# Kernel tuning notes

Measured on AMD Instinct MI355X. Metric: run time of the kernel, lower is better.

## Reference

```python
import jax, jax.numpy as jnp
import numpy as np

D_MODEL = 2048
N_HEADS = 16
HEAD_DIM = D_MODEL // N_HEADS  # 128
B, T = 2, 1024
XL_LEN = 1024


def setup_inputs() -> dict:
    key = jax.random.key(0)
    ks = jax.random.split(key, 8)
    # rotary angles for head_dim/2 pairs (llama-style)
    inv_freq = 1.0 / (10000.0 ** (jnp.arange(0, HEAD_DIM, 2, dtype=jnp.float32) / HEAD_DIM))
    t = jnp.arange(T, dtype=jnp.float32)
    freqs = jnp.outer(t, inv_freq)  # [T, HEAD_DIM//2]
    return {
        "x": jax.random.normal(ks[0], (B, T, D_MODEL), dtype=jnp.float32),
        "cos": jnp.cos(freqs),
        "sin": jnp.sin(freqs),
        "k_xl": jax.random.normal(ks[1], (B, XL_LEN, D_MODEL), dtype=jnp.float32),
        "v_xl": jax.random.normal(ks[2], (B, XL_LEN, D_MODEL), dtype=jnp.float32),
        "pos_emb": jax.random.normal(ks[3], (XL_LEN, D_MODEL), dtype=jnp.float32) * 0.02,
        "w_qkv": jax.random.normal(ks[4], (3 * D_MODEL, D_MODEL), dtype=jnp.float32) * 0.02,
        "w_proj": jax.random.normal(ks[5], (D_MODEL, D_MODEL), dtype=jnp.float32) * 0.02,
        "is_causal": 0,
    }


def _apply_rope(x, cos, sin):
    # x: [B, T, H, hd]; cos/sin: [T, hd//2]
    xr = x.reshape(*x.shape[:-1], HEAD_DIM // 2, 2)
    x1, x2 = xr[..., 0], xr[..., 1]
    c = cos[None, :, None, :]
    s = sin[None, :, None, :]
    o1 = x1 * c - x2 * s
    o2 = x1 * s + x2 * c
    return jnp.stack([o1, o2], axis=-1).reshape(x.shape)


def reference(x, cos, sin, k_xl, v_xl, pos_emb, w_qkv, w_proj, is_causal):
    Bq, Tq, C = x.shape
    H, hd = N_HEADS, HEAD_DIM
    qkv = jnp.einsum('btc,fc->btf', x, w_qkv)  # fused QKV projection
    q, k, v = jnp.split(qkv, 3, axis=-1)
    # add learned XL positional embedding to cached keys (self.k_xl += emb(arange))
    k_xl = k_xl + pos_emb[None, :, :]
    q = q.reshape(Bq, Tq, H, hd)
    k = k.reshape(Bq, -1, H, hd)
    v = v.reshape(Bq, -1, H, hd)
    q = _apply_rope(q, cos, sin)
    k = _apply_rope(k, cos, sin)
    q = q.transpose(0, 2, 1, 3)  # [B,H,T,hd]
    k = k.transpose(0, 2, 1, 3)
    v = v.transpose(0, 2, 1, 3)
    k_xl_h = k_xl.reshape(Bq, -1, H, hd).transpose(0, 2, 1, 3)
    v_xl_h = v_xl.reshape(Bq, -1, H, hd).transpose(0, 2, 1, 3)
    k_full = jnp.concatenate([k_xl_h, k], axis=-2)  # [B,H,XL+T,hd]
    v_full = jnp.concatenate([v_xl_h, v], axis=-2)
    scale = 1.0 / jnp.sqrt(jnp.asarray(hd, dtype=q.dtype))
    scores = jnp.einsum('bhqd,bhkd->bhqk', q, k_full) * scale
    if is_causal:
        Kv = k_full.shape[-2]
        qi = jnp.arange(Tq)[:, None]
        ki = jnp.arange(Kv)[None, :]
        scores = jnp.where(ki <= qi + (Kv - Tq), scores, jnp.finfo(scores.dtype).min)
    attn = jax.nn.softmax(scores, axis=-1)
    y = jnp.einsum('bhqk,bhkd->bhqd', attn, v_full)
    y = y.transpose(0, 2, 1, 3).reshape(Bq, Tq, C)
    return jnp.einsum('btc,oc->bto', y, w_proj)
```

## Files before the change

kernel.cpp:

```cpp
#include <hip/hip_runtime.h>
#include <stdint.h>

typedef unsigned short u16;
typedef __attribute__((ext_vector_type(4))) float f32x4;
typedef __attribute__((ext_vector_type(8))) short bf16x8;
typedef __attribute__((ext_vector_type(4))) uint32_t u32x4;

#define D_MODEL 2048
#define NHEADS 16
#define HD 128
#define BSZ 2
#define TQ 1024
#define XL 1024
#define KVLEN 2048

__device__ __forceinline__ float b2f(u16 u) {
  union { uint32_t i; float f; } x; x.i = ((uint32_t)u) << 16; return x.f;
}
__device__ __forceinline__ u16 f2b(float f) {
  union { float f; uint32_t i; } x; x.f = f;
  uint32_t r = x.i + 0x7FFFu + ((x.i >> 16) & 1u);
  return (u16)(r >> 16);
}

union U4 { u32x4 u; u16 s[8]; };

__device__ __forceinline__ void async_copy16(const u16* g, u16* l) {
  __builtin_amdgcn_global_load_lds((__attribute__((address_space(1))) void*)g,
                                   (__attribute__((address_space(3))) void*)l,
                                   16, 0, 0);
}

__device__ __forceinline__ float rmax16(float v) {
  v = fmaxf(v, __shfl_xor(v, 1));
  v = fmaxf(v, __shfl_xor(v, 2));
  v = fmaxf(v, __shfl_xor(v, 4));
  v = fmaxf(v, __shfl_xor(v, 8));
  return v;
}
__device__ __forceinline__ float rsum16(float v) {
  v += __shfl_xor(v, 1);
  v += __shfl_xor(v, 2);
  v += __shfl_xor(v, 4);
  v += __shfl_xor(v, 8);
  return v;
}

struct PrefF32 {
  f32x4 lo, hi;
  __device__ __forceinline__ void load(const float* base, size_t off) {
    lo = *(const f32x4*)(base + off);
    hi = *(const f32x4*)(base + off + 4);
  }
  __device__ __forceinline__ u32x4 pack() const {
    U4 o;
    o.s[0] = f2b(lo[0]); o.s[1] = f2b(lo[1]); o.s[2] = f2b(lo[2]); o.s[3] = f2b(lo[3]);
    o.s[4] = f2b(hi[0]); o.s[5] = f2b(hi[1]); o.s[6] = f2b(hi[2]); o.s[7] = f2b(hi[3]);
    return o.u;
  }
};

__global__ __launch_bounds__(256, 4) void cvt_bf16(
    const float* __restrict__ src, u16* __restrict__ dst)
{
  const size_t id = (size_t)blockIdx.x * 256 + threadIdx.x;
  PrefF32 p; p.load(src, id * 8);
  *(u32x4*)&dst[id * 8] = p.pack();
}

template <int BN, bool CSPLIT>
__global__ __launch_bounds__(256, 2) void gemm_bt(
    const u16* __restrict__ A, const u16* __restrict__ B,
    void* __restrict__ C0, void* __restrict__ C1, void* __restrict__ C2,
    int M, int N, int K)
{
  constexpr int JN = BN / 32;
  __shared__ u16 sA[128 * 32];
  __shared__ u16 sB[BN * 32];
  const int tid  = threadIdx.x;
  const int lane = tid & 63;
  const int wave = tid >> 6;
  const int quad = lane >> 4;
  const int mcol = lane & 15;
  const int wm = (wave >> 1) * 64;
  const int wn = (wave & 1) * (BN / 2);
  const int bm = blockIdx.y * 128;
  const int bnE = blockIdx.x * BN;

  f32x4 acc[4][JN] = {};

  const int c0 = tid, c1 = tid + 256;
  size_t a0 = (size_t)(bm + (c0 >> 2)) * K + (c0 & 3) * 8;
  size_t a1 = (size_t)(bm + (c1 >> 2)) * K + (c1 & 3) * 8;
  size_t b0 = (size_t)(bnE + (c0 >> 2)) * K + (c0 & 3) * 8;
  size_t b1 = (BN == 128) ? (size_t)(bnE + (c1 >> 2)) * K + (c1 & 3) * 8 : 0;

  const int nk = K >> 5;
  for (int kk = 0; kk < nk; ++kk) {
    async_copy16(A + a0, &sA[c0 * 8]);
    async_copy16(A + a1, &sA[c1 * 8]);
    async_copy16(B + b0, &sB[c0 * 8]);
    if (BN == 128) async_copy16(B + b1, &sB[c1 * 8]);
    a0 += 32; a1 += 32; b0 += 32; b1 += 32;
    __syncthreads();
    bf16x8 af[4], bff[JN];
#pragma unroll
    for (int i = 0; i < 4; ++i)
      af[i] = *(const bf16x8*)&sA[(wm + i * 16 + mcol) * 32 + quad * 8];
#pragma unroll
    for (int j = 0; j < JN; ++j)
      bff[j] = *(const bf16x8*)&sB[(wn + j * 16 + mcol) * 32 + quad * 8];
#pragma unroll
    for (int i = 0; i < 4; ++i)
#pragma unroll
      for (int j = 0; j < JN; ++j)
        acc[i][j] = __builtin_amdgcn_mfma_f32_16x16x32_bf16(af[i], bff[j], acc[i][j], 0, 0, 0);
    __syncthreads();
  }

  if (CSPLIT) {
    const int sel = bnE >> 11;
    u16* Cp = (u16*)(sel == 0 ? C0 : (sel == 1 ? C1 : C2));
    const int bnl = (bnE & 2047) + wn;
#pragma unroll
    for (int i = 0; i < 4; ++i)
#pragma unroll
      for (int r = 0; r < 4; ++r) {
        const size_t base = (size_t)(bm + wm + i * 16 + quad * 4 + r) * 2048 + bnl;
#pragma unroll
        for (int j = 0; j < JN; ++j)
          Cp[base + j * 16 + mcol] = f2b(acc[i][j][r]);
      }
  } else {
    float* Cp = (float*)C0;
#pragma unroll
    for (int i = 0; i < 4; ++i)
#pragma unroll
      for (int r = 0; r < 4; ++r) {
        const size_t base = (size_t)(bm + wm + i * 16 + quad * 4 + r) * N + bnE + wn;
#pragma unroll
        for (int j = 0; j < JN; ++j)
          Cp[base + j * 16 + mcol] = acc[i][j][r];
      }
  }
}

__global__ __launch_bounds__(256, 4) void prep_k(
    const float* __restrict__ kxl, const float* __restrict__ pos,
    const u16* __restrict__ kbuf, const float* __restrict__ cosw,
    const float* __restrict__ sinw, u16* __restrict__ kfull)
{
  const int id = blockIdx.x * 256 + threadIdx.x;
  const int dc = id & 15;
  const int kv = (id >> 4) & 2047;
  const int bh = id >> 15;
  const int b = bh >> 4, h = bh & 15;
  const int d0 = dc * 8;
  U4 o;
  if (kv < XL) {
    const float* kp = kxl + ((size_t)b * XL + kv) * D_MODEL + h * HD + d0;
    const float* pp = pos + (size_t)kv * D_MODEL + h * HD + d0;
    f32x4 kl = *(const f32x4*)kp, kh = *(const f32x4*)(kp + 4);
    f32x4 pl = *(const f32x4*)pp, ph = *(const f32x4*)(pp + 4);
#pragma unroll
    for (int p = 0; p < 4; ++p) {
      o.s[p]     = f2b(kl[p] + pl[p]);
      o.s[4 + p] = f2b(kh[p] + ph[p]);
    }
  } else {
    const int tq = kv - XL;
    U4 kv_;
    kv_.u = *(const u32x4*)(kbuf + ((size_t)b * TQ + tq) * D_MODEL + h * HD + d0);
    f32x4 cv = *(const f32x4*)(cosw + tq * 64 + (d0 >> 1));
    f32x4 sv = *(const f32x4*)(sinw + tq * 64 + (d0 >> 1));
#pragma unroll
    for (int p = 0; p < 4; ++p) {
      const float e = b2f(kv_.s[2 * p]), od = b2f(kv_.s[2 * p + 1]);
      o.s[2 * p]     = f2b(e * cv[p] - od * sv[p]);
      o.s[2 * p + 1] = f2b(e * sv[p] + od * cv[p]);
    }
  }
  *(u32x4*)&kfull[((size_t)bh * KVLEN + kv) * HD + d0] = o.u;
}

__global__ __launch_bounds__(256, 4) void transpose_v(
    const float* __restrict__ v_xl, const u16* __restrict__ vbuf, u16* __restrict__ vt)
{
  __shared__ u16 tile[64 * 72];
  const int tid = threadIdx.x;
  const int kv0 = blockIdx.x * 64;
  const int d0  = blockIdx.y * 64;
  const int bh  = blockIdx.z;
  const int b = bh >> 4, h = bh & 15;
#pragma unroll
  for (int j = 0; j < 2; ++j) {
    const int id = tid + 256 * j;
    const int kr = id >> 3, dq = (id & 7) * 8;
    const int kvg = kv0 + kr;
    if (kvg < XL) {
      const float* src = v_xl + ((size_t)b * XL + kvg) * D_MODEL + h * HD + d0 + dq;
      PrefF32 p; p.load(src, 0);
      *(u32x4*)&tile[kr * 72 + dq] = p.pack();
    } else {
      const u16* src = vbuf + ((size_t)b * TQ + (kvg - XL)) * D_MODEL + h * HD + d0 + dq;
      *(u32x4*)&tile[kr * 72 + dq] = *(const u32x4*)src;
    }
  }
  __syncthreads();
#pragma unroll
  for (int j = 0; j < 2; ++j) {
    const int id = tid + 256 * j;
    const int dr = id >> 3, kq = (id & 7) * 8;
    U4 ov;
#pragma unroll
    for (int i = 0; i < 8; ++i) ov.s[i] = tile[(kq + i) * 72 + dr];
    *(u32x4*)&vt[((size_t)bh * HD + d0 + dr) * KVLEN + kv0 + kq] = ov.u;
  }
}

#define LSTR 136

__global__ __launch_bounds__(256, 2) void attn(
    const u16* __restrict__ q, const u16* __restrict__ kfull,
    const u16* __restrict__ vt, const float* __restrict__ cosw,
    const float* __restrict__ sinw, const int* __restrict__ iscausal,
    u16* __restrict__ y)
{
  __shared__ u16 sK[128 * LSTR];
  __shared__ u16 sV[128 * LSTR];

  const int tid  = threadIdx.x;
  const int lane = tid & 63;
  const int w    = tid >> 6;
  const int quad = lane >> 4;
  const int mcol = lane & 15;
  const int qt = blockIdx.x;
  const int bh = blockIdx.y;
  const int b = bh >> 4, h = bh & 15;
  const int causal = *iscausal;
  const float SC = 0.08838834764831845f;

  bf16x8 qf[4];
  {
    const int trow = qt * 64 + w * 16 + mcol;
    const u16* qrow = q + ((size_t)b * TQ + trow) * D_MODEL + h * HD;
    const float* crow = cosw + trow * 64;
    const float* srow = sinw + trow * 64;
#pragma unroll
    for (int ks = 0; ks < 4; ++ks) {
      const int d0 = ks * 32 + quad * 8;
      U4 qv; qv.u = *(const u32x4*)(qrow + d0);
      f32x4 cv = *(const f32x4*)(crow + (d0 >> 1));
      f32x4 sv = *(const f32x4*)(srow + (d0 >> 1));
      bf16x8 dst;
#pragma unroll
      for (int p = 0; p < 4; ++p) {
        const float e = b2f(qv.s[2 * p]), o = b2f(qv.s[2 * p + 1]);
        dst[2 * p]     = (short)f2b((e * cv[p] - o * sv[p]) * SC);
        dst[2 * p + 1] = (short)f2b((e * sv[p] + o * cv[p]) * SC);
      }
      qf[ks] = dst;
    }
  }

  const int srow = tid >> 4;
  const int sc8 = (tid & 15) * 8;
  const u16* kbase = kfull + (size_t)bh * KVLEN * HD;
  const u16* vbase = vt + (size_t)bh * HD * KVLEN;

  u32x4 kreg[8], vreg[8];
#define LOADT(KV0)                                                          \
  do {                                                                      \
    _Pragma("unroll") for (int j = 0; j < 8; ++j) {                         \
      const int rr = srow + 16 * j;                                         \
      kreg[j] = *(const u32x4*)(kbase + ((size_t)(KV0) + rr) * HD + sc8);   \
      vreg[j] = *(const u32x4*)(vbase + (size_t)rr * KVLEN + (KV0) + sc8);  \
    }                                                                       \
  } while (0)

  f32x4 oacc[8] = {};
  float mrun[4], lrun[4];
#pragma unroll
  for (int r = 0; r < 4; ++r) { mrun[r] = -3.0e38f; lrun[r] = 0.f; }

  LOADT(0);
  for (int t16 = 0; t16 < 16; ++t16) {
    __syncthreads();
#pragma unroll
    for (int j = 0; j < 8; ++j) {
      const int rr = srow + 16 * j;
      *(u32x4*)&sK[rr * LSTR + sc8] = kreg[j];
      *(u32x4*)&sV[rr * LSTR + sc8] = vreg[j];
    }
    __syncthreads();
    if (t16 < 15) LOADT((t16 + 1) * 128);

    const int kv0 = t16 * 128;

    f32x4 s[8] = {};
#pragma unroll
    for (int ks = 0; ks < 4; ++ks) {
      const int cc = ks * 4 + quad;
#pragma unroll
      for (int nt = 0; nt < 8; ++nt) {
        bf16x8 kf = *(const bf16x8*)&sK[(nt * 16 + mcol) * LSTR + cc * 8];
        s[nt] = __builtin_amdgcn_mfma_f32_16x16x32_bf16(qf[ks], kf, s[nt], 0, 0, 0);
      }
    }
    if (causal) {
#pragma unroll
      for (int r = 0; r < 4; ++r) {
        const int qi = qt * 64 + w * 16 + quad * 4 + r;
#pragma unroll
        for (int nt = 0; nt < 8; ++nt) {
          const int ki = kv0 + nt * 16 + mcol;
          if (ki > qi + (KVLEN - TQ)) s[nt][r] = -1.0e30f;
        }
      }
    }

#pragma unroll
    for (int r = 0; r < 4; ++r) {
      float tm = -3.0e38f;
#pragma unroll
      for (int nt = 0; nt < 8; ++nt) tm = fmaxf(tm, s[nt][r]);
      tm = rmax16(tm);
      const float mo = mrun[r];
      const float mn = fmaxf(mo, tm);
      mrun[r] = mn;
      const float al = __expf(mo - mn);
      float rs = 0.f;
#pragma unroll
      for (int nt = 0; nt < 8; ++nt) {
        const float p = __expf(s[nt][r] - mn);
        s[nt][r] = p;
        rs += p;
      }
      rs = rsum16(rs);
      lrun[r] = lrun[r] * al + rs;
#pragma unroll
      for (int nd = 0; nd < 8; ++nd) oacc[nd][r] *= al;
    }
    __syncthreads();

    u16* sPw = &sK[w * 16 * LSTR];
#pragma unroll
    for (int r = 0; r < 4; ++r) {
      const int row = quad * 4 + r;
#pragma unroll
      for (int nt = 0; nt < 8; ++nt)
        sPw[row * LSTR + nt * 16 + mcol] = f2b(s[nt][r]);
    }

#pragma unroll
    for (int ks = 0; ks < 4; ++ks) {
      const int cc = ks * 4 + quad;
      bf16x8 pa = *(const bf16x8*)&sPw[mcol * LSTR + cc * 8];
#pragma unroll
      for (int nd = 0; nd < 8; ++nd) {
        bf16x8 vf = *(const bf16x8*)&sV[(nd * 16 + mcol) * LSTR + cc * 8];
        oacc[nd] = __builtin_amdgcn_mfma_f32_16x16x32_bf16(pa, vf, oacc[nd], 0, 0, 0);
      }
    }
  }
#undef LOADT

#pragma unroll
  for (int r = 0; r < 4; ++r) {
    const int trow = qt * 64 + w * 16 + quad * 4 + r;
    const float inv = 1.0f / lrun[r];
    u16* yr = y + ((size_t)b * TQ + trow) * D_MODEL + h * HD;
#pragma unroll
    for (int nd = 0; nd < 8; ++nd)
      yr[nd * 16 + mcol] = f2b(oacc[nd][r] * inv);
  }
}

extern "C" void kernel_launch(void* const* d_in, const int* in_sizes, int n_in,
                              void* d_out, int out_size, void* d_ws, size_t ws_size,
                              hipStream_t stream) {
  const float* x      = (const float*)d_in[0];
  const float* cosw   = (const float*)d_in[1];
  const float* sinw   = (const float*)d_in[2];
  const float* k_xl   = (const float*)d_in[3];
  const float* v_xl   = (const float*)d_in[4];
  const float* pos    = (const float*)d_in[5];
  const float* w_qkv  = (const float*)d_in[6];
  const float* w_proj = (const float*)d_in[7];
  const int* isc      = (const int*)d_in[8];
  float* out = (float*)d_out;

  char* ws = (char*)d_ws;
  u16* qbuf  = (u16*)ws;
  u16* kbuf  = (u16*)(ws + (size_t)8388608);
  u16* vbuf  = (u16*)(ws + (size_t)16777216);
  u16* wqb   = (u16*)(ws + (size_t)25165824);
  u16* kfull = (u16*)(ws + (size_t)25165824);
  u16* wpb   = (u16*)(ws + (size_t)25165824);
  u16* vt    = (u16*)(ws + (size_t)41943040);
  u16* xb    = (u16*)(ws + (size_t)50331648);
  u16* y_ws  = kbuf;

  cvt_bf16<<<2048, 256, 0, stream>>>(x, xb);
  cvt_bf16<<<6144, 256, 0, stream>>>(w_qkv, wqb);

  dim3 g1(48, 16);
  gemm_bt<128, true><<<g1, 256, 0, stream>>>(xb, wqb, qbuf, kbuf, vbuf, 2048, 6144, 2048);

  prep_k<<<4096, 256, 0, stream>>>(k_xl, pos, kbuf, cosw, sinw, kfull);

  dim3 gt(KVLEN / 64, HD / 64, BSZ * NHEADS);
  transpose_v<<<gt, 256, 0, stream>>>(v_xl, vbuf, vt);

  dim3 ga(16, BSZ * NHEADS);
  attn<<<ga, 256, 0, stream>>>(qbuf, kfull, vt, cosw, sinw, isc, y_ws);

  cvt_bf16<<<2048, 256, 0, stream>>>(w_proj, wpb);

  dim3 g2(32, 16);
  gemm_bt<64, false><<<g2, 256, 0, stream>>>(y_ws, wpb, out, nullptr, nullptr, 2048, 2048, 2048);
}
```

Measured before the change: 351.2 us.

## Split attention KV tile across wave pairs with lazy rescale and MFMA row sums

The attention kernel now runs 512 threads per block, with two waves per 16-query slice, each owning half of every 128-key tile. Their partial softmax states are merged through shared memory at the end. The kernel also skips rescaling unless the running max grows by more than a threshold, computes row sums with an MFMA against a ones vector instead of shuffle reductions, and raises wave priority around MFMA sections. The goal is more waves in flight to hide latency with only 512 blocks, at the cost of a final merge step, extra barriers, and more work per row sum.

```diff
diff --git a/kernel.cpp b/kernel.cpp
--- a/kernel.cpp
+++ b/kernel.cpp
@@ -36,13 +36,6 @@
   v = fmaxf(v, __shfl_xor(v, 2));
   v = fmaxf(v, __shfl_xor(v, 4));
   v = fmaxf(v, __shfl_xor(v, 8));
-  return v;
-}
-__device__ __forceinline__ float rsum16(float v) {
-  v += __shfl_xor(v, 1);
-  v += __shfl_xor(v, 2);
-  v += __shfl_xor(v, 4);
-  v += __shfl_xor(v, 8);
   return v;
 }
 
@@ -220,7 +213,7 @@
 
 #define LSTR 136
 
-__global__ __launch_bounds__(256, 2) void attn(
+__global__ __launch_bounds__(512, 4) void attn(
     const u16* __restrict__ q, const u16* __restrict__ kfull,
     const u16* __restrict__ vt, const float* __restrict__ cosw,
     const float* __restrict__ sinw, const int* __restrict__ iscausal,
@@ -232,6 +225,8 @@
   const int tid  = threadIdx.x;
   const int lane = tid & 63;
   const int w    = tid >> 6;
+  const int qw   = w >> 1;
+  const int kh   = w & 1;
   const int quad = lane >> 4;
   const int mcol = lane & 15;
   const int qt = blockIdx.x;
@@ -242,16 +237,16 @@
 
   bf16x8 qf[4];
   {
-    const int trow = qt * 64 + w * 16 + mcol;
+    const int trow = qt * 64 + qw * 16 + mcol;
     const u16* qrow = q + ((size_t)b * TQ + trow) * D_MODEL + h * HD;
     const float* crow = cosw + trow * 64;
-    const float* srow = sinw + trow * 64;
+    const float* srow_ = sinw + trow * 64;
 #pragma unroll
     for (int ks = 0; ks < 4; ++ks) {
       const int d0 = ks * 32 + quad * 8;
       U4 qv; qv.u = *(const u32x4*)(qrow + d0);
       f32x4 cv = *(const f32x4*)(crow + (d0 >> 1));
-      f32x4 sv = *(const f32x4*)(srow + (d0 >> 1));
+      f32x4 sv = *(const f32x4*)(srow_ + (d0 >> 1));
       bf16x8 dst;
 #pragma unroll
       for (int p = 0; p < 4; ++p) {
@@ -263,32 +258,37 @@
     }
   }
 
+  bf16x8 onesf;
+#pragma unroll
+  for (int p = 0; p < 8; ++p) onesf[p] = (short)0x3F80;
+
   const int srow = tid >> 4;
   const int sc8 = (tid & 15) * 8;
   const u16* kbase = kfull + (size_t)bh * KVLEN * HD;
   const u16* vbase = vt + (size_t)bh * HD * KVLEN;
 
-  u32x4 kreg[8], vreg[8];
+  u32x4 kreg[4], vreg[4];
 #define LOADT(KV0)                                                          \
   do {                                                                      \
-    _Pragma("unroll") for (int j = 0; j < 8; ++j) {                         \
-      const int rr = srow + 16 * j;                                         \
+    _Pragma("unroll") for (int j = 0; j < 4; ++j) {                         \
+      const int rr = srow + 32 * j;                                         \
       kreg[j] = *(const u32x4*)(kbase + ((size_t)(KV0) + rr) * HD + sc8);   \
       vreg[j] = *(const u32x4*)(vbase + (size_t)rr * KVLEN + (KV0) + sc8);  \
     }                                                                       \
   } while (0)
 
   f32x4 oacc[8] = {};
-  float mrun[4], lrun[4];
-#pragma unroll
-  for (int r = 0; r < 4; ++r) { mrun[r] = -3.0e38f; lrun[r] = 0.f; }
+  f32x4 lacc = {};
+  float mrun[4];
+#pragma unroll
+  for (int r = 0; r < 4; ++r) mrun[r] = -3.0e38f;
 
   LOADT(0);
   for (int t16 = 0; t16 < 16; ++t16) {
     __syncthreads();
 #pragma unroll
-    for (int j = 0; j < 8; ++j) {
-      const int rr = srow + 16 * j;
+    for (int j = 0; j < 4; ++j) {
+      const int rr = srow + 32 * j;
       *(u32x4*)&sK[rr * LSTR + sc8] = kreg[j];
       *(u32x4*)&sV[rr * LSTR + sc8] = vreg[j];
     }
@@ -297,23 +297,25 @@
 
     const int kv0 = t16 * 128;
 
-    f32x4 s[8] = {};
+    f32x4 s[4] = {};
+    __builtin_amdgcn_s_setprio(1);
 #pragma unroll
     for (int ks = 0; ks < 4; ++ks) {
       const int cc = ks * 4 + quad;
 #pragma unroll
-      for (int nt = 0; nt < 8; ++nt) {
-        bf16x8 kf = *(const bf16x8*)&sK[(nt * 16 + mcol) * LSTR + cc * 8];
+      for (int nt = 0; nt < 4; ++nt) {
+        bf16x8 kf = *(const bf16x8*)&sK[(kh * 64 + nt * 16 + mcol) * LSTR + cc * 8];
         s[nt] = __builtin_amdgcn_mfma_f32_16x16x32_bf16(qf[ks], kf, s[nt], 0, 0, 0);
       }
     }
+    __builtin_amdgcn_s_setprio(0);
     if (causal) {
 #pragma unroll
       for (int r = 0; r < 4; ++r) {
-        const int qi = qt * 64 + w * 16 + quad * 4 + r;
-#pragma unroll
-        for (int nt = 0; nt < 8; ++nt) {
-          const int ki = kv0 + nt * 16 + mcol;
+        const int qi = qt * 64 + qw * 16 + quad * 4 + r;
+#pragma unroll
+        for (int nt = 0; nt < 4; ++nt) {
+          const int ki = kv0 + kh * 64 + nt * 16 + mcol;
           if (ki > qi + (KVLEN - TQ)) s[nt][r] = -1.0e30f;
         }
       }
@@ -321,25 +323,19 @@
 
 #pragma unroll
     for (int r = 0; r < 4; ++r) {
-      float tm = -3.0e38f;
-#pragma unroll
-      for (int nt = 0; nt < 8; ++nt) tm = fmaxf(tm, s[nt][r]);
+      float tm = fmaxf(fmaxf(s[0][r], s[1][r]), fmaxf(s[2][r], s[3][r]));
       tm = rmax16(tm);
       const float mo = mrun[r];
-      const float mn = fmaxf(mo, tm);
-      mrun[r] = mn;
-      const float al = __expf(mo - mn);
-      float rs = 0.f;
-#pragma unroll
-      for (int nt = 0; nt < 8; ++nt) {
-        const float p = __expf(s[nt][r] - mn);
-        s[nt][r] = p;
-        rs += p;
-      }
-      rs = rsum16(rs);
-      lrun[r] = lrun[r] * al + rs;
-#pragma unroll
-      for (int nd = 0; nd < 8; ++nd) oacc[nd][r] *= al;
+      const float mn = (tm <= mo + 8.0f) ? mo : tm;
+#pragma unroll
+      for (int nt = 0; nt < 4; ++nt) s[nt][r] = __expf(s[nt][r] - mn);
+      if (mn != mo) {
+        const float al = __expf(mo - mn);
+#pragma unroll
+        for (int nd = 0; nd < 8; ++nd) oacc[nd][r] *= al;
+        lacc[r] *= al;
+        mrun[r] = mn;
+      }
     }
     __syncthreads();
 
@@ -348,31 +344,66 @@
     for (int r = 0; r < 4; ++r) {
       const int row = quad * 4 + r;
 #pragma unroll
-      for (int nt = 0; nt < 8; ++nt)
+      for (int nt = 0; nt < 4; ++nt)
         sPw[row * LSTR + nt * 16 + mcol] = f2b(s[nt][r]);
     }
 
-#pragma unroll
-    for (int ks = 0; ks < 4; ++ks) {
+    __builtin_amdgcn_s_setprio(1);
+#pragma unroll
+    for (int ks = 0; ks < 2; ++ks) {
       const int cc = ks * 4 + quad;
       bf16x8 pa = *(const bf16x8*)&sPw[mcol * LSTR + cc * 8];
+      lacc = __builtin_amdgcn_mfma_f32_16x16x32_bf16(pa, onesf, lacc, 0, 0, 0);
 #pragma unroll
       for (int nd = 0; nd < 8; ++nd) {
-        bf16x8 vf = *(const bf16x8*)&sV[(nd * 16 + mcol) * LSTR + cc * 8];
+        bf16x8 vf = *(const bf16x8*)&sV[(nd * 16 + mcol) * LSTR + kh * 64 + cc * 8];
         oacc[nd] = __builtin_amdgcn_mfma_f32_16x16x32_bf16(pa, vf, oacc[nd], 0, 0, 0);
       }
     }
+    __builtin_amdgcn_s_setprio(0);
   }
 #undef LOADT
 
-#pragma unroll
-  for (int r = 0; r < 4; ++r) {
-    const int trow = qt * 64 + w * 16 + quad * 4 + r;
-    const float inv = 1.0f / lrun[r];
-    u16* yr = y + ((size_t)b * TQ + trow) * D_MODEL + h * HD;
-#pragma unroll
-    for (int nd = 0; nd < 8; ++nd)
-      yr[nd * 16 + mcol] = f2b(oacc[nd][r] * inv);
+  __syncthreads();
+  float* mO  = (float*)sK;
+  float* mML = (float*)sV;
+  if (kh) {
+#pragma unroll
+    for (int r = 0; r < 4; ++r) {
+      const int row = quad * 4 + r;
+#pragma unroll
+      for (int nd = 0; nd < 8; ++nd)
+        mO[(qw * 16 + row) * 128 + nd * 16 + mcol] = oacc[nd][r];
+    }
+    if (mcol == 0) {
+#pragma unroll
+      for (int r = 0; r < 4; ++r) {
+        const int row = quad * 4 + r;
+        mML[(qw * 16 + row) * 2 + 0] = mrun[r];
+        mML[(qw * 16 + row) * 2 + 1] = lacc[r];
+      }
+    }
+  }
+  __syncthreads();
+  if (!kh) {
+#pragma unroll
+    for (int r = 0; r < 4; ++r) {
+      const int row = quad * 4 + r;
+      const int trow = qt * 64 + qw * 16 + row;
+      const float m1 = mML[(qw * 16 + row) * 2 + 0];
+      const float l1 = mML[(qw * 16 + row) * 2 + 1];
+      const float m  = fmaxf(mrun[r], m1);
+      const float f0 = __expf(mrun[r] - m);
+      const float f1 = __expf(m1 - m);
+      const float inv = 1.0f / (lacc[r] * f0 + l1 * f1);
+      u16* yr = y + ((size_t)b * TQ + trow) * D_MODEL + h * HD;
+#pragma unroll
+      for (int nd = 0; nd < 8; ++nd) {
+        const float o0 = oacc[nd][r];
+        const float o1 = mO[(qw * 16 + row) * 128 + nd * 16 + mcol];
+        yr[nd * 16 + mcol] = f2b((o0 * f0 + o1 * f1) * inv);
+      }
+    }
   }
 }
 
@@ -413,7 +444,7 @@
   transpose_v<<<gt, 256, 0, stream>>>(v_xl, vbuf, vt);
 
   dim3 ga(16, BSZ * NHEADS);
-  attn<<<ga, 256, 0, stream>>>(qbuf, kfull, vt, cosw, sinw, isc, y_ws);
+  attn<<<ga, 512, 0, stream>>>(qbuf, kfull, vt, cosw, sinw, isc, y_ws);
 
   cvt_bf16<<<2048, 256, 0, stream>>>(w_proj, wpb);
 
```

After: 387.3 us. +10.3%, slower.

## Compute softmax row sums via MFMA and skip rescaling with lazy max threshold

Applied to the files above, without the earlier changes.

Changes the attention kernel's online softmax. The row-sum accumulation and its shuffle reduction are replaced by an extra MFMA of P against a ones vector. The running max is updated only when the new tile max exceeds the old one by more than 8, so the rescaling of the output accumulator runs only when needed. The patch also adds s_setprio around the MFMA blocks and uses fmaf in the query RoPE. The lazy max lets exponentials grow up to e^8 before rescaling, and the row sum is now formed from bf16-rounded probabilities, which slightly changes numerics.

```diff
diff --git a/kernel.cpp b/kernel.cpp
--- a/kernel.cpp
+++ b/kernel.cpp
@@ -36,13 +36,6 @@
   v = fmaxf(v, __shfl_xor(v, 2));
   v = fmaxf(v, __shfl_xor(v, 4));
   v = fmaxf(v, __shfl_xor(v, 8));
-  return v;
-}
-__device__ __forceinline__ float rsum16(float v) {
-  v += __shfl_xor(v, 1);
-  v += __shfl_xor(v, 2);
-  v += __shfl_xor(v, 4);
-  v += __shfl_xor(v, 8);
   return v;
 }
 
@@ -256,12 +249,18 @@
 #pragma unroll
       for (int p = 0; p < 4; ++p) {
         const float e = b2f(qv.s[2 * p]), o = b2f(qv.s[2 * p + 1]);
-        dst[2 * p]     = (short)f2b((e * cv[p] - o * sv[p]) * SC);
-        dst[2 * p + 1] = (short)f2b((e * sv[p] + o * cv[p]) * SC);
+        const float re = fmaf(-o, sv[p], e * cv[p]);
+        const float im = fmaf( o, cv[p], e * sv[p]);
+        dst[2 * p]     = (short)f2b(re * SC);
+        dst[2 * p + 1] = (short)f2b(im * SC);
       }
       qf[ks] = dst;
     }
   }
+
+  bf16x8 onesf;
+#pragma unroll
+  for (int p = 0; p < 8; ++p) onesf[p] = (short)0x3F80;
 
   const int srow = tid >> 4;
   const int sc8 = (tid & 15) * 8;
@@ -279,9 +278,10 @@
   } while (0)
 
   f32x4 oacc[8] = {};
-  float mrun[4], lrun[4];
-#pragma unroll
-  for (int r = 0; r < 4; ++r) { mrun[r] = -3.0e38f; lrun[r] = 0.f; }
+  f32x4 lacc = {};
+  float mrun[4];
+#pragma unroll
+  for (int r = 0; r < 4; ++r) mrun[r] = -3.0e38f;
 
   LOADT(0);
   for (int t16 = 0; t16 < 16; ++t16) {
@@ -298,6 +298,7 @@
     const int kv0 = t16 * 128;
 
     f32x4 s[8] = {};
+    __builtin_amdgcn_s_setprio(1);
 #pragma unroll
     for (int ks = 0; ks < 4; ++ks) {
       const int cc = ks * 4 + quad;
@@ -307,6 +308,7 @@
         s[nt] = __builtin_amdgcn_mfma_f32_16x16x32_bf16(qf[ks], kf, s[nt], 0, 0, 0);
       }
     }
+    __builtin_amdgcn_s_setprio(0);
     if (causal) {
 #pragma unroll
       for (int r = 0; r < 4; ++r) {
@@ -321,25 +323,20 @@
 
 #pragma unroll
     for (int r = 0; r < 4; ++r) {
-      float tm = -3.0e38f;
-#pragma unroll
-      for (int nt = 0; nt < 8; ++nt) tm = fmaxf(tm, s[nt][r]);
+      float tm = fmaxf(fmaxf(fmaxf(s[0][r], s[1][r]), fmaxf(s[2][r], s[3][r])),
+                       fmaxf(fmaxf(s[4][r], s[5][r]), fmaxf(s[6][r], s[7][r])));
       tm = rmax16(tm);
       const float mo = mrun[r];
-      const float mn = fmaxf(mo, tm);
-      mrun[r] = mn;
-      const float al = __expf(mo - mn);
-      float rs = 0.f;
-#pragma unroll
-      for (int nt = 0; nt < 8; ++nt) {
-        const float p = __expf(s[nt][r] - mn);
-        s[nt][r] = p;
-        rs += p;
-      }
-      rs = rsum16(rs);
-      lrun[r] = lrun[r] * al + rs;
-#pragma unroll
-      for (int nd = 0; nd < 8; ++nd) oacc[nd][r] *= al;
+      const float mn = (tm <= mo + 8.0f) ? mo : tm;
+#pragma unroll
+      for (int nt = 0; nt < 8; ++nt) s[nt][r] = __expf(s[nt][r] - mn);
+      if (mn != mo) {
+        const float al = __expf(mo - mn);
+#pragma unroll
+        for (int nd = 0; nd < 8; ++nd) oacc[nd][r] *= al;
+        lacc[r] *= al;
+        mrun[r] = mn;
+      }
     }
     __syncthreads();
 
@@ -352,23 +349,26 @@
         sPw[row * LSTR + nt * 16 + mcol] = f2b(s[nt][r]);
     }
 
+    __builtin_amdgcn_s_setprio(1);
 #pragma unroll
     for (int ks = 0; ks < 4; ++ks) {
       const int cc = ks * 4 + quad;
       bf16x8 pa = *(const bf16x8*)&sPw[mcol * LSTR + cc * 8];
+      lacc = __builtin_amdgcn_mfma_f32_16x16x32_bf16(pa, onesf, lacc, 0, 0, 0);
 #pragma unroll
       for (int nd = 0; nd < 8; ++nd) {
         bf16x8 vf = *(const bf16x8*)&sV[(nd * 16 + mcol) * LSTR + cc * 8];
         oacc[nd] = __builtin_amdgcn_mfma_f32_16x16x32_bf16(pa, vf, oacc[nd], 0, 0, 0);
       }
     }
+    __builtin_amdgcn_s_setprio(0);
   }
 #undef LOADT
 
 #pragma unroll
   for (int r = 0; r < 4; ++r) {
     const int trow = qt * 64 + w * 16 + quad * 4 + r;
-    const float inv = 1.0f / lrun[r];
+    const float inv = 1.0f / lacc[r];
     u16* yr = y + ((size_t)b * TQ + trow) * D_MODEL + h * HD;
 #pragma unroll
     for (int nd = 0; nd < 8; ++nd)
```

Measured after the change: 359.2 us. +2.3%, slower.
